# Optimization experiments

Hardware: AMD Instinct MI355X
Metric: run time of the kernel (lower is better)

## Reference

```python
import jax, jax.numpy as jnp
import numpy as np

B, T, E, H = 256, 1024, 32, 128
N_OBS = 1048576
N_OBS_VOCAB = 11  # n_lands + 2
N_ACT_VOCAB = 5   # n_acts + 2


def setup_inputs() -> dict:
    key = jax.random.key(0)
    ks = jax.random.split(key, 10)
    obs_ids = jax.random.randint(ks[0], (N_OBS,), 0, N_OBS_VOCAB)
    obs_slot = jnp.sort(jax.random.randint(ks[1], (N_OBS,), 0, B * T))
    action_ids = jax.random.randint(ks[2], (B, T), 0, N_ACT_VOCAB)
    is_action = jax.random.bernoulli(ks[3], 0.5, (B, T))
    lengths = jax.random.randint(ks[4], (B,), T // 4, T + 1)
    input_lengths = jnp.sort(lengths)[::-1]  # pack_padded_sequence requires descending
    s = 1.0 / np.sqrt(H)
    action_emb = jax.random.normal(ks[5], (N_ACT_VOCAB, E), jnp.float32)
    obs_emb = jax.random.normal(ks[6], (N_OBS_VOCAB, E), jnp.float32)
    W_ih = jax.random.uniform(ks[7], (4 * H, E), jnp.float32, -s, s)
    W_hh = jax.random.uniform(ks[8], (4 * H, H), jnp.float32, -s, s)
    b_ih = jax.random.uniform(ks[9], (4 * H,), jnp.float32, -s, s)
    b_hh = jnp.zeros((4 * H,), jnp.float32)
    return dict(obs_ids=obs_ids, obs_slot=obs_slot, action_ids=action_ids,
                is_action=is_action, input_lengths=input_lengths,
                action_emb=action_emb, obs_emb=obs_emb,
                W_ih=W_ih, W_hh=W_hh, b_ih=b_ih, b_hh=b_hh)


def _embed(obs_ids, obs_slot, action_ids, is_action, action_emb, obs_emb):
    # fused ragged embedding-bag: gather + segment-sum over observation lists
    obs_sum = jax.ops.segment_sum(obs_emb[obs_ids], obs_slot, num_segments=B * T)
    obs_sum = obs_sum.reshape(B, T, E)
    act = action_emb[action_ids]  # [B,T,E]
    return jnp.where(is_action[..., None], act, obs_sum)


def _lstm(embedded, input_lengths, W_ih, W_hh, b_ih, b_hh):
    mask = (jnp.arange(T)[None, :] < input_lengths[:, None])  # [B,T]
    xs = jnp.swapaxes(embedded, 0, 1)                         # [T,B,E]
    ms = mask.T[..., None].astype(embedded.dtype)             # [T,B,1]

    def step(carry, inp):
        h, c = carry
        x, m = inp
        gates = x @ W_ih.T + h @ W_hh.T + (b_ih + b_hh)  # [B,4H]
        i, f, g, o = jnp.split(gates, 4, axis=-1)        # torch gate order i,f,g,o
        i, f, o = jax.nn.sigmoid(i), jax.nn.sigmoid(f), jax.nn.sigmoid(o)
        g = jnp.tanh(g)
        c_new = f * c + i * g
        h_new = o * jnp.tanh(c_new)
        h = m * h_new + (1.0 - m) * h  # frozen past length (packed semantics)
        c = m * c_new + (1.0 - m) * c
        return (h, c), h * m           # pad_packed zero-pads past length

    h0 = jnp.zeros((B, H), embedded.dtype)
    c0 = jnp.zeros((B, H), embedded.dtype)
    (hN, cN), outs = jax.lax.scan(step, (h0, c0), (xs, ms))
    return jnp.swapaxes(outs, 0, 1), hN[None], cN[None]  # outputs [B,T,H], h/c [1,B,H]


def reference(obs_ids, obs_slot, action_ids, is_action, input_lengths,
              action_emb, obs_emb, W_ih, W_hh, b_ih, b_hh):
    embedded = _embed(obs_ids, obs_slot, action_ids, is_action, action_emb, obs_emb)
    outputs, h, c = _lstm(embedded, input_lengths, W_ih, W_hh, b_ih, b_hh)
    return outputs, h, c, embedded
```

## Files before the change

### kernel.cpp

```cpp
#include <hip/hip_runtime.h>

#define B_ 256
#define T_ 1024
#define E_ 32
#define H_ 128
#define NOBS_ 1048576
#define L2E 1.4426950408889634f
#define CLM 30.0f

#define HROW 144
#define HBUF (4 * HROW)

typedef __attribute__((ext_vector_type(8))) short bf16x8;
typedef __attribute__((ext_vector_type(4))) float f32x4;
typedef __attribute__((ext_vector_type(4))) int   i32x4;

#define LDS_BARRIER() asm volatile("s_waitcnt lgkmcnt(0)\n\ts_barrier" ::: "memory")

__device__ __forceinline__ short f2bf(float x) {
    unsigned u = __float_as_uint(x);
    unsigned r = u + 0x7FFFu + ((u >> 16) & 1u);
    return (short)(r >> 16);
}

__device__ __forceinline__ bf16x8 pack8(float4 lo, float4 hi) {
    int x0, x1, x2, x3;
    asm("v_cvt_pk_bf16_f32 %0, %1, %2" : "=v"(x0) : "v"(lo.x), "v"(lo.y));
    asm("v_cvt_pk_bf16_f32 %0, %1, %2" : "=v"(x1) : "v"(lo.z), "v"(lo.w));
    asm("v_cvt_pk_bf16_f32 %0, %1, %2" : "=v"(x2) : "v"(hi.x), "v"(hi.y));
    asm("v_cvt_pk_bf16_f32 %0, %1, %2" : "=v"(x3) : "v"(hi.z), "v"(hi.w));
    i32x4 xi; xi[0] = x0; xi[1] = x1; xi[2] = x2; xi[3] = x3;
    return __builtin_bit_cast(bf16x8, xi);
}

__global__ void embed_kernel(const int* __restrict__ obs_ids,
                             const int* __restrict__ obs_slot,
                             const int* __restrict__ action_ids,
                             const int* __restrict__ is_action,
                             const float* __restrict__ action_emb,
                             const float* __restrict__ obs_emb,
                             float* __restrict__ embedded,
                             unsigned short* __restrict__ xbf) {
    __shared__ float s_act[5 * E_];
    __shared__ float s_obs[11 * E_];
    for (int i = threadIdx.x; i < 5 * E_; i += blockDim.x) s_act[i] = action_emb[i];
    for (int i = threadIdx.x; i < 11 * E_; i += blockDim.x) s_obs[i] = obs_emb[i];
    __syncthreads();

    int s = blockIdx.x * blockDim.x + threadIdx.x;
    if (s >= B_ * T_) return;

    float acc[E_];
    if (is_action[s]) {
        int a = action_ids[s];
        #pragma unroll
        for (int e = 0; e < E_; e++) acc[e] = s_act[a * E_ + e];
    } else {
        #pragma unroll
        for (int e = 0; e < E_; e++) acc[e] = 0.0f;
        int lo = 0, hi = NOBS_;
        while (lo < hi) {
            int mid = (lo + hi) >> 1;
            if (obs_slot[mid] < s) lo = mid + 1; else hi = mid;
        }
        int j = lo;
        while (j < NOBS_ && obs_slot[j] == s) {
            int id = obs_ids[j];
            #pragma unroll
            for (int e = 0; e < E_; e++) acc[e] += s_obs[id * E_ + e];
            j++;
        }
    }
    float4* dst = (float4*)(embedded + (size_t)s * E_);
    #pragma unroll
    for (int q = 0; q < E_ / 4; q++) {
        float4 v; v.x = acc[4*q]; v.y = acc[4*q+1]; v.z = acc[4*q+2]; v.w = acc[4*q+3];
        dst[q] = v;
    }
    if (xbf) {
        unsigned short tmp[E_];
        #pragma unroll
        for (int e = 0; e < E_; e++) tmp[e] = (unsigned short)f2bf(acc[e]);
        int4* d2 = (int4*)(xbf + (size_t)s * E_);
        #pragma unroll
        for (int q = 0; q < E_ / 8; q++) d2[q] = ((const int4*)tmp)[q];
    }
}

template<bool BF16X>
__launch_bounds__(512, 2)
__global__ void lstm_kernel(const float* __restrict__ embedded,
                            const unsigned short* __restrict__ xbf,
                            const int* __restrict__ lengths,
                            const float* __restrict__ W_ih,
                            const float* __restrict__ W_hh,
                            const float* __restrict__ b_ih,
                            const float* __restrict__ b_hh,
                            float* __restrict__ outputs,
                            float* __restrict__ h_out,
                            float* __restrict__ c_out) {
    __shared__ __align__(16) char h_lds[2 * HBUF];

    const int tid  = threadIdx.x;
    const int lane = tid & 63;
    const int wave = tid >> 6;
    const int row0 = blockIdx.x * 4;

    const int col16  = (wave << 4) + (lane & 15);
    const int kgrp8  = (lane >> 4) * 8;
    const int kgrp16 = (lane >> 4) * 16;
    const int brow   = (lane & 15) >> 2;
    const int g_own  = lane >> 4;

    bf16x8 wx[4]; f32x4 biasv[4]; i32x4 wh[4][2]; float dq[4];
    #pragma unroll
    for (int gt = 0; gt < 4; gt++) {
        const float scale = (gt == 2) ? (2.0f * L2E) : L2E;
        const int gcol = gt * H_ + col16;
        {
            const float* p = W_ih + (size_t)gcol * E_ + kgrp8;
            bf16x8 v;
            #pragma unroll
            for (int j = 0; j < 8; j++) v[j] = f2bf(p[j] * scale);
            wx[gt] = v;
        }
        biasv[gt] = (f32x4)((b_ih[gcol] + b_hh[gcol]) * scale);

        const float* q = W_hh + (size_t)gcol * H_;
        float m = 0.0f;
        #pragma unroll
        for (int t2 = 0; t2 < 2; t2++)
            #pragma unroll
            for (int j = 0; j < 16; j++)
                m = fmaxf(m, fabsf(q[t2 * 64 + kgrp16 + j]));
        m = fmaxf(m, __shfl_xor(m, 16));
        m = fmaxf(m, __shfl_xor(m, 32));
        const float s = 127.0f / m;
        dq[gt] = scale * m * (1.0f / (127.0f * 127.0f));
        #pragma unroll
        for (int t2 = 0; t2 < 2; t2++) {
            i32x4 v;
            #pragma unroll
            for (int d = 0; d < 4; d++) {
                int word = 0;
                #pragma unroll
                for (int b2 = 0; b2 < 4; b2++) {
                    int qi = (int)rintf(q[t2 * 64 + kgrp16 + d * 4 + b2] * s);
                    word |= (qi & 0xFF) << (b2 * 8);
                }
                v[d] = word;
            }
            wh[gt][t2] = v;
        }
    }

    const int len = lengths[row0 + g_own];
    float cr = 0.0f, hr = 0.0f;

    const unsigned short* xpb = xbf + ((size_t)(row0 + brow) * T_) * E_ + kgrp8;
    const float*          xpf = embedded + ((size_t)(row0 + brow) * T_) * E_ + kgrp8;

    const int rbase = brow * HROW + kgrp16;
    const int wofs  = g_own * HROW + col16;
    float* const out_base = outputs + (size_t)(row0 + g_own) * T_ * H_ + col16;

    for (int i = tid; i < 2 * HBUF; i += 512) h_lds[i] = 0;
    __syncthreads();

    int4 xfA, xfB;
    float4 flA, fhA, flB, fhB;
    auto loadx = [&](int t, int4& xi4, float4& fl, float4& fh) {
        if (BF16X) {
            xi4 = *(const int4*)(xpb + (size_t)t * E_);
        } else {
            fl = *(const float4*)(xpf + (size_t)t * E_);
            fh = *(const float4*)(xpf + (size_t)t * E_ + 4);
        }
    };
    auto mkfrag = [&](const int4& xi4, const float4& fl, const float4& fh) -> bf16x8 {
        if (BF16X) return __builtin_bit_cast(bf16x8, xi4);
        return pack8(fl, fh);
    };

    loadx(0, xfA, flA, fhA);
    loadx(1, xfB, flB, fhB);
    f32x4 accfA[4], accfB[4];
    {
        bf16x8 xa = mkfrag(xfA, flA, fhA);
        #pragma unroll
        for (int gt = 0; gt < 4; gt++)
            accfA[gt] = __builtin_amdgcn_mfma_f32_16x16x32_bf16(xa, wx[gt], biasv[gt], 0, 0, 0);
    }

    auto step = [&](int t, int RD, int WR,
                    f32x4* accf_cur, f32x4* accf_nxt,
                    const int4& xf_nx, const float4& fl_nx, const float4& fh_nx,
                    int4& xf_pf, float4& fl_pf, float4& fh_pf,
                    bool PF1, bool PF2) {
        i32x4 ah0 = *(const i32x4*)&h_lds[RD + rbase];
        i32x4 ah1 = *(const i32x4*)&h_lds[RD + rbase + 64];

        if (PF2) loadx(t + 2, xf_pf, fl_pf, fh_pf);

        __builtin_amdgcn_s_setprio(1);
        i32x4 acci[4];
        #pragma unroll
        for (int gt = 0; gt < 4; gt++)
            acci[gt] = __builtin_amdgcn_mfma_i32_16x16x64_i8(ah0, wh[gt][0], (i32x4)0, 0, 0, 0);
        #pragma unroll
        for (int gt = 0; gt < 4; gt++)
            acci[gt] = __builtin_amdgcn_mfma_i32_16x16x64_i8(ah1, wh[gt][1], acci[gt], 0, 0, 0);
        if (PF1) {
            bf16x8 xa = mkfrag(xf_nx, fl_nx, fh_nx);
            #pragma unroll
            for (int gt = 0; gt < 4; gt++)
                accf_nxt[gt] = __builtin_amdgcn_mfma_f32_16x16x32_bf16(xa, wx[gt], biasv[gt], 0, 0, 0);
        }
        __builtin_amdgcn_s_setprio(0);

        float a_i = fmaf((float)acci[0][0], dq[0], accf_cur[0][0]);
        float a_f = fmaf((float)acci[1][0], dq[1], accf_cur[1][0]);
        float a_g = fmaf((float)acci[2][0], dq[2], accf_cur[2][0]);
        float a_o = fmaf((float)acci[3][0], dq[3], accf_cur[3][0]);
        float Ai = exp2f(fminf(-a_i, CLM));
        float Af = exp2f(fminf(-a_f, CLM));
        float Eg = exp2f(fminf(a_g, CLM));
        float pAi = 1.0f + Ai, pAf = 1.0f + Af, pEg = Eg + 1.0f;
        float D  = pAi * pEg;
        float R  = __builtin_amdgcn_rcpf(D * pAf);
        float f_ = D * R;
        float ig = (Eg - 1.0f) * pAf * R;
        float c_new = fmaf(f_, cr, ig);
        float Ec = exp2f(fminf(c_new * (2.0f * L2E), CLM));
        float Ao = exp2f(fminf(-a_o, CLM));
        float Rh = __builtin_amdgcn_rcpf((1.0f + Ao) * (Ec + 1.0f));
        float h_new = (Ec - 1.0f) * Rh;
        bool m = (t < len);
        cr = m ? c_new : cr;
        hr = m ? h_new : hr;

        unsigned qb = __float_as_uint(fmaf(hr, 127.0f, 12582912.0f));
        h_lds[WR + wofs] = (char)qb;
        out_base[(size_t)t * H_] = m ? h_new : 0.0f;

        LDS_BARRIER();
    };

    for (int t = 0; t < T_ - 2; t += 2) {
        step(t,     0,    HBUF, accfA, accfB, xfB, flB, fhB, xfA, flA, fhA, true, true);
        step(t + 1, HBUF, 0,    accfB, accfA, xfA, flA, fhA, xfB, flB, fhB, true, t + 3 < T_);
    }
    step(T_ - 2, 0,    HBUF, accfA, accfB, xfB, flB, fhB, xfA, flA, fhA, true,  false);
    step(T_ - 1, HBUF, 0,    accfB, accfA, xfA, flA, fhA, xfB, flB, fhB, false, false);

    h_out[(size_t)(row0 + g_own) * H_ + col16] = hr;
    c_out[(size_t)(row0 + g_own) * H_ + col16] = cr;
}

extern "C" void kernel_launch(void* const* d_in, const int* in_sizes, int n_in,
                              void* d_out, int out_size, void* d_ws, size_t ws_size,
                              hipStream_t stream) {
    const int*   obs_ids       = (const int*)d_in[0];
    const int*   obs_slot      = (const int*)d_in[1];
    const int*   action_ids    = (const int*)d_in[2];
    const int*   is_action     = (const int*)d_in[3];
    const int*   input_lengths = (const int*)d_in[4];
    const float* action_emb    = (const float*)d_in[5];
    const float* obs_emb       = (const float*)d_in[6];
    const float* W_ih          = (const float*)d_in[7];
    const float* W_hh          = (const float*)d_in[8];
    const float* b_ih          = (const float*)d_in[9];
    const float* b_hh          = (const float*)d_in[10];

    float* out      = (float*)d_out;
    float* outputs  = out;
    float* h_out    = out + (size_t)B_ * T_ * H_;
    float* c_out    = h_out + (size_t)B_ * H_;
    float* embedded = c_out + (size_t)B_ * H_;

    const size_t xbf_bytes = (size_t)B_ * T_ * E_ * sizeof(unsigned short);
    const bool use_bf16x = (ws_size >= xbf_bytes);
    unsigned short* xbf = use_bf16x ? (unsigned short*)d_ws : nullptr;

    hipLaunchKernelGGL(embed_kernel, dim3((B_ * T_ + 255) / 256), dim3(256), 0, stream,
                       obs_ids, obs_slot, action_ids, is_action, action_emb, obs_emb,
                       embedded, xbf);

    if (use_bf16x) {
        hipLaunchKernelGGL((lstm_kernel<true>), dim3(B_ / 4), dim3(512), 0, stream,
                           embedded, xbf, input_lengths, W_ih, W_hh, b_ih, b_hh,
                           outputs, h_out, c_out);
    } else {
        hipLaunchKernelGGL((lstm_kernel<false>), dim3(B_ / 4), dim3(512), 0, stream,
                           embedded, xbf, input_lengths, W_ih, W_hh, b_ih, b_hh,
                           outputs, h_out, c_out);
    }
}
```

Before: 487.3 us.

## Run one batch row per LSTM block instead of four

Changes the LSTM kernel so that each 512-thread block handles a single batch row, launching 256 blocks instead of 64. This spreads the serial recurrence across more CUs to use more of the GPU. It also removes the software pipelining of the input projection, which is now computed inside the same step. Only 16 lanes per wave write results, so most MFMA rows do wasted work, and the per-step latency chain now includes the x-projection MFMAs.

```diff
diff --git a/kernel.cpp b/kernel.cpp
--- a/kernel.cpp
+++ b/kernel.cpp
@@ -8,8 +8,7 @@
 #define L2E 1.4426950408889634f
 #define CLM 30.0f
 
-#define HROW 144
-#define HBUF (4 * HROW)
+#define HR1 144
 
 typedef __attribute__((ext_vector_type(8))) short bf16x8;
 typedef __attribute__((ext_vector_type(4))) float f32x4;
@@ -88,29 +87,27 @@
 }
 
 template<bool BF16X>
-__launch_bounds__(512, 2)
-__global__ void lstm_kernel(const float* __restrict__ embedded,
-                            const unsigned short* __restrict__ xbf,
-                            const int* __restrict__ lengths,
-                            const float* __restrict__ W_ih,
-                            const float* __restrict__ W_hh,
-                            const float* __restrict__ b_ih,
-                            const float* __restrict__ b_hh,
-                            float* __restrict__ outputs,
-                            float* __restrict__ h_out,
-                            float* __restrict__ c_out) {
-    __shared__ __align__(16) char h_lds[2 * HBUF];
+__launch_bounds__(512)
+__global__ void lstm1_kernel(const float* __restrict__ embedded,
+                             const unsigned short* __restrict__ xbf,
+                             const int* __restrict__ lengths,
+                             const float* __restrict__ W_ih,
+                             const float* __restrict__ W_hh,
+                             const float* __restrict__ b_ih,
+                             const float* __restrict__ b_hh,
+                             float* __restrict__ outputs,
+                             float* __restrict__ h_out,
+                             float* __restrict__ c_out) {
+    __shared__ __align__(16) char h_lds[2 * HR1];
 
     const int tid  = threadIdx.x;
     const int lane = tid & 63;
     const int wave = tid >> 6;
-    const int row0 = blockIdx.x * 4;
+    const int row  = blockIdx.x;
 
     const int col16  = (wave << 4) + (lane & 15);
     const int kgrp8  = (lane >> 4) * 8;
     const int kgrp16 = (lane >> 4) * 16;
-    const int brow   = (lane & 15) >> 2;
-    const int g_own  = lane >> 4;
 
     bf16x8 wx[4]; f32x4 biasv[4]; i32x4 wh[4][2]; float dq[4];
     #pragma unroll
@@ -154,17 +151,14 @@
         }
     }
 
-    const int len = lengths[row0 + g_own];
+    const int len = lengths[row];
     float cr = 0.0f, hr = 0.0f;
 
-    const unsigned short* xpb = xbf + ((size_t)(row0 + brow) * T_) * E_ + kgrp8;
-    const float*          xpf = embedded + ((size_t)(row0 + brow) * T_) * E_ + kgrp8;
-
-    const int rbase = brow * HROW + kgrp16;
-    const int wofs  = g_own * HROW + col16;
-    float* const out_base = outputs + (size_t)(row0 + g_own) * T_ * H_ + col16;
-
-    for (int i = tid; i < 2 * HBUF; i += 512) h_lds[i] = 0;
+    const unsigned short* xpb = xbf + (size_t)row * T_ * E_ + kgrp8;
+    const float*          xpf = embedded + (size_t)row * T_ * E_ + kgrp8;
+    float* const out_base = outputs + (size_t)row * T_ * H_ + col16;
+
+    for (int i = tid; i < 2 * HR1; i += 512) h_lds[i] = 0;
     __syncthreads();
 
     int4 xfA, xfB;
@@ -184,44 +178,35 @@
 
     loadx(0, xfA, flA, fhA);
     loadx(1, xfB, flB, fhB);
-    f32x4 accfA[4], accfB[4];
-    {
-        bf16x8 xa = mkfrag(xfA, flA, fhA);
+
+    int RD = 0;
+    for (int t = 0; t < T_; ++t) {
+        const int cur = t & 1;
+        i32x4 ah0 = *(const i32x4*)&h_lds[RD + kgrp16];
+        i32x4 ah1 = *(const i32x4*)&h_lds[RD + 64 + kgrp16];
+        bf16x8 xa = mkfrag(cur ? xfB : xfA, cur ? flB : flA, cur ? fhB : fhA);
+        if (t + 2 < T_) {
+            if (cur) loadx(t + 2, xfB, flB, fhB);
+            else     loadx(t + 2, xfA, flA, fhA);
+        }
+
+        __builtin_amdgcn_s_setprio(1);
+        f32x4 accf[4]; i32x4 acci[4];
         #pragma unroll
         for (int gt = 0; gt < 4; gt++)
-            accfA[gt] = __builtin_amdgcn_mfma_f32_16x16x32_bf16(xa, wx[gt], biasv[gt], 0, 0, 0);
-    }
-
-    auto step = [&](int t, int RD, int WR,
-                    f32x4* accf_cur, f32x4* accf_nxt,
-                    const int4& xf_nx, const float4& fl_nx, const float4& fh_nx,
-                    int4& xf_pf, float4& fl_pf, float4& fh_pf,
-                    bool PF1, bool PF2) {
-        i32x4 ah0 = *(const i32x4*)&h_lds[RD + rbase];
-        i32x4 ah1 = *(const i32x4*)&h_lds[RD + rbase + 64];
-
-        if (PF2) loadx(t + 2, xf_pf, fl_pf, fh_pf);
-
-        __builtin_amdgcn_s_setprio(1);
-        i32x4 acci[4];
+            accf[gt] = __builtin_amdgcn_mfma_f32_16x16x32_bf16(xa, wx[gt], biasv[gt], 0, 0, 0);
         #pragma unroll
         for (int gt = 0; gt < 4; gt++)
             acci[gt] = __builtin_amdgcn_mfma_i32_16x16x64_i8(ah0, wh[gt][0], (i32x4)0, 0, 0, 0);
         #pragma unroll
         for (int gt = 0; gt < 4; gt++)
             acci[gt] = __builtin_amdgcn_mfma_i32_16x16x64_i8(ah1, wh[gt][1], acci[gt], 0, 0, 0);
-        if (PF1) {
-            bf16x8 xa = mkfrag(xf_nx, fl_nx, fh_nx);
-            #pragma unroll
-            for (int gt = 0; gt < 4; gt++)
-                accf_nxt[gt] = __builtin_amdgcn_mfma_f32_16x16x32_bf16(xa, wx[gt], biasv[gt], 0, 0, 0);
-        }
         __builtin_amdgcn_s_setprio(0);
 
-        float a_i = fmaf((float)acci[0][0], dq[0], accf_cur[0][0]);
-        float a_f = fmaf((float)acci[1][0], dq[1], accf_cur[1][0]);
-        float a_g = fmaf((float)acci[2][0], dq[2], accf_cur[2][0]);
-        float a_o = fmaf((float)acci[3][0], dq[3], accf_cur[3][0]);
+        float a_i = fmaf((float)acci[0][0], dq[0], accf[0][0]);
+        float a_f = fmaf((float)acci[1][0], dq[1], accf[1][0]);
+        float a_g = fmaf((float)acci[2][0], dq[2], accf[2][0]);
+        float a_o = fmaf((float)acci[3][0], dq[3], accf[3][0]);
         float Ai = exp2f(fminf(-a_i, CLM));
         float Af = exp2f(fminf(-a_f, CLM));
         float Eg = exp2f(fminf(a_g, CLM));
@@ -239,22 +224,20 @@
         cr = m ? c_new : cr;
         hr = m ? h_new : hr;
 
-        unsigned qb = __float_as_uint(fmaf(hr, 127.0f, 12582912.0f));
-        h_lds[WR + wofs] = (char)qb;
-        out_base[(size_t)t * H_] = m ? h_new : 0.0f;
-
+        const int WR = RD ^ HR1;
+        if (lane < 16) {
+            unsigned qb = __float_as_uint(fmaf(hr, 127.0f, 12582912.0f));
+            h_lds[WR + col16] = (char)qb;
+            out_base[(size_t)t * H_] = m ? h_new : 0.0f;
+        }
+        RD = WR;
         LDS_BARRIER();
-    };
-
-    for (int t = 0; t < T_ - 2; t += 2) {
-        step(t,     0,    HBUF, accfA, accfB, xfB, flB, fhB, xfA, flA, fhA, true, true);
-        step(t + 1, HBUF, 0,    accfB, accfA, xfA, flA, fhA, xfB, flB, fhB, true, t + 3 < T_);
-    }
-    step(T_ - 2, 0,    HBUF, accfA, accfB, xfB, flB, fhB, xfA, flA, fhA, true,  false);
-    step(T_ - 1, HBUF, 0,    accfB, accfA, xfA, flA, fhA, xfB, flB, fhB, false, false);
-
-    h_out[(size_t)(row0 + g_own) * H_ + col16] = hr;
-    c_out[(size_t)(row0 + g_own) * H_ + col16] = cr;
+    }
+
+    if (lane < 16) {
+        h_out[(size_t)row * H_ + col16] = hr;
+        c_out[(size_t)row * H_ + col16] = cr;
+    }
 }
 
 extern "C" void kernel_launch(void* const* d_in, const int* in_sizes, int n_in,
@@ -287,11 +270,11 @@
                        embedded, xbf);
 
     if (use_bf16x) {
-        hipLaunchKernelGGL((lstm_kernel<true>), dim3(B_ / 4), dim3(512), 0, stream,
+        hipLaunchKernelGGL((lstm1_kernel<true>), dim3(B_), dim3(512), 0, stream,
                            embedded, xbf, input_lengths, W_ih, W_hh, b_ih, b_hh,
                            outputs, h_out, c_out);
     } else {
-        hipLaunchKernelGGL((lstm_kernel<false>), dim3(B_ / 4), dim3(512), 0, stream,
+        hipLaunchKernelGGL((lstm1_kernel<false>), dim3(B_), dim3(512), 0, stream,
                            embedded, xbf, input_lengths, W_ih, W_hh, b_ih, b_hh,
                            outputs, h_out, c_out);
     }
```

Measured after the change: 747.9 us. +53.5%, slower.

## Batch input projection over four timesteps per MFMA using all accumulator rows

Applied to the files above, without the earlier changes.

The input projection MFMA previously produced 16 rows but only row 0 of each accumulator was used, so one x-projection ran per timestep. Each lane now loads the input for timestep offset (lane&3), so one bf16 MFMA yields the projections for four consecutive timesteps, indexed by accf[gt][i]. This cuts the x-projection MFMAs and global loads per step by four and prefetches eight steps ahead. The trade-off is that the projection is no longer overlapped inside the recurrent step and accumulators are held across four steps.

```diff
diff --git a/kernel.cpp b/kernel.cpp
--- a/kernel.cpp
+++ b/kernel.cpp
@@ -110,6 +110,7 @@
     const int kgrp8  = (lane >> 4) * 8;
     const int kgrp16 = (lane >> 4) * 16;
     const int brow   = (lane & 15) >> 2;
+    const int toff   = (lane & 15) & 3;
     const int g_own  = lane >> 4;
 
     bf16x8 wx[4]; f32x4 biasv[4]; i32x4 wh[4][2]; float dq[4];
@@ -157,8 +158,8 @@
     const int len = lengths[row0 + g_own];
     float cr = 0.0f, hr = 0.0f;
 
-    const unsigned short* xpb = xbf + ((size_t)(row0 + brow) * T_) * E_ + kgrp8;
-    const float*          xpf = embedded + ((size_t)(row0 + brow) * T_) * E_ + kgrp8;
+    const unsigned short* xpb = xbf + ((size_t)(row0 + brow) * T_ + toff) * E_ + kgrp8;
+    const float*          xpf = embedded + ((size_t)(row0 + brow) * T_ + toff) * E_ + kgrp8;
 
     const int rbase = brow * HROW + kgrp16;
     const int wofs  = g_own * HROW + col16;
@@ -167,14 +168,14 @@
     for (int i = tid; i < 2 * HBUF; i += 512) h_lds[i] = 0;
     __syncthreads();
 
-    int4 xfA, xfB;
-    float4 flA, fhA, flB, fhB;
-    auto loadx = [&](int t, int4& xi4, float4& fl, float4& fh) {
+    int4 xf0, xf1;
+    float4 fl0, fh0, fl1, fh1;
+    auto loadx = [&](int tg, int4& xi4, float4& fl, float4& fh) {
         if (BF16X) {
-            xi4 = *(const int4*)(xpb + (size_t)t * E_);
+            xi4 = *(const int4*)(xpb + (size_t)tg * E_);
         } else {
-            fl = *(const float4*)(xpf + (size_t)t * E_);
-            fh = *(const float4*)(xpf + (size_t)t * E_ + 4);
+            fl = *(const float4*)(xpf + (size_t)tg * E_);
+            fh = *(const float4*)(xpf + (size_t)tg * E_ + 4);
         }
     };
     auto mkfrag = [&](const int4& xi4, const float4& fl, const float4& fh) -> bf16x8 {
@@ -182,76 +183,72 @@
         return pack8(fl, fh);
     };
 
-    loadx(0, xfA, flA, fhA);
-    loadx(1, xfB, flB, fhB);
-    f32x4 accfA[4], accfB[4];
-    {
-        bf16x8 xa = mkfrag(xfA, flA, fhA);
+    loadx(0, xf0, fl0, fh0);
+    loadx(4, xf1, fl1, fh1);
+
+    auto group = [&](int tg, const int4& xf_u, const float4& fl_u, const float4& fh_u,
+                     int4& xf_p, float4& fl_p, float4& fh_p, bool PF) {
+        bf16x8 xa = mkfrag(xf_u, fl_u, fh_u);
+        f32x4 accf[4];
+        __builtin_amdgcn_s_setprio(1);
         #pragma unroll
         for (int gt = 0; gt < 4; gt++)
-            accfA[gt] = __builtin_amdgcn_mfma_f32_16x16x32_bf16(xa, wx[gt], biasv[gt], 0, 0, 0);
-    }
-
-    auto step = [&](int t, int RD, int WR,
-                    f32x4* accf_cur, f32x4* accf_nxt,
-                    const int4& xf_nx, const float4& fl_nx, const float4& fh_nx,
-                    int4& xf_pf, float4& fl_pf, float4& fh_pf,
-                    bool PF1, bool PF2) {
-        i32x4 ah0 = *(const i32x4*)&h_lds[RD + rbase];
-        i32x4 ah1 = *(const i32x4*)&h_lds[RD + rbase + 64];
-
-        if (PF2) loadx(t + 2, xf_pf, fl_pf, fh_pf);
-
-        __builtin_amdgcn_s_setprio(1);
-        i32x4 acci[4];
-        #pragma unroll
-        for (int gt = 0; gt < 4; gt++)
-            acci[gt] = __builtin_amdgcn_mfma_i32_16x16x64_i8(ah0, wh[gt][0], (i32x4)0, 0, 0, 0);
-        #pragma unroll
-        for (int gt = 0; gt < 4; gt++)
-            acci[gt] = __builtin_amdgcn_mfma_i32_16x16x64_i8(ah1, wh[gt][1], acci[gt], 0, 0, 0);
-        if (PF1) {
-            bf16x8 xa = mkfrag(xf_nx, fl_nx, fh_nx);
+            accf[gt] = __builtin_amdgcn_mfma_f32_16x16x32_bf16(xa, wx[gt], biasv[gt], 0, 0, 0);
+        __builtin_amdgcn_s_setprio(0);
+        if (PF) loadx(tg + 8, xf_p, fl_p, fh_p);
+
+        #pragma unroll
+        for (int i = 0; i < 4; i++) {
+            const int t  = tg + i;
+            const int RD = (i & 1) ? HBUF : 0;
+            const int WR = RD ^ HBUF;
+
+            i32x4 ah0 = *(const i32x4*)&h_lds[RD + rbase];
+            i32x4 ah1 = *(const i32x4*)&h_lds[RD + rbase + 64];
+
+            __builtin_amdgcn_s_setprio(1);
+            i32x4 acci[4];
             #pragma unroll
             for (int gt = 0; gt < 4; gt++)
-                accf_nxt[gt] = __builtin_amdgcn_mfma_f32_16x16x32_bf16(xa, wx[gt], biasv[gt], 0, 0, 0);
-        }
-        __builtin_amdgcn_s_setprio(0);
-
-        float a_i = fmaf((float)acci[0][0], dq[0], accf_cur[0][0]);
-        float a_f = fmaf((float)acci[1][0], dq[1], accf_cur[1][0]);
-        float a_g = fmaf((float)acci[2][0], dq[2], accf_cur[2][0]);
-        float a_o = fmaf((float)acci[3][0], dq[3], accf_cur[3][0]);
-        float Ai = exp2f(fminf(-a_i, CLM));
-        float Af = exp2f(fminf(-a_f, CLM));
-        float Eg = exp2f(fminf(a_g, CLM));
-        float pAi = 1.0f + Ai, pAf = 1.0f + Af, pEg = Eg + 1.0f;
-        float D  = pAi * pEg;
-        float R  = __builtin_amdgcn_rcpf(D * pAf);
-        float f_ = D * R;
-        float ig = (Eg - 1.0f) * pAf * R;
-        float c_new = fmaf(f_, cr, ig);
-        float Ec = exp2f(fminf(c_new * (2.0f * L2E), CLM));
-        float Ao = exp2f(fminf(-a_o, CLM));
-        float Rh = __builtin_amdgcn_rcpf((1.0f + Ao) * (Ec + 1.0f));
-        float h_new = (Ec - 1.0f) * Rh;
-        bool m = (t < len);
-        cr = m ? c_new : cr;
-        hr = m ? h_new : hr;
-
-        unsigned qb = __float_as_uint(fmaf(hr, 127.0f, 12582912.0f));
-        h_lds[WR + wofs] = (char)qb;
-        out_base[(size_t)t * H_] = m ? h_new : 0.0f;
-
-        LDS_BARRIER();
+                acci[gt] = __builtin_amdgcn_mfma_i32_16x16x64_i8(ah0, wh[gt][0], (i32x4)0, 0, 0, 0);
+            #pragma unroll
+            for (int gt = 0; gt < 4; gt++)
+                acci[gt] = __builtin_amdgcn_mfma_i32_16x16x64_i8(ah1, wh[gt][1], acci[gt], 0, 0, 0);
+            __builtin_amdgcn_s_setprio(0);
+
+            float a_i = fmaf((float)acci[0][0], dq[0], accf[0][i]);
+            float a_f = fmaf((float)acci[1][0], dq[1], accf[1][i]);
+            float a_g = fmaf((float)acci[2][0], dq[2], accf[2][i]);
+            float a_o = fmaf((float)acci[3][0], dq[3], accf[3][i]);
+            float Ai = exp2f(fminf(-a_i, CLM));
+            float Af = exp2f(fminf(-a_f, CLM));
+            float Eg = exp2f(fminf(a_g, CLM));
+            float pAi = 1.0f + Ai, pAf = 1.0f + Af, pEg = Eg + 1.0f;
+            float D  = pAi * pEg;
+            float R  = __builtin_amdgcn_rcpf(D * pAf);
+            float f_ = D * R;
+            float ig = (Eg - 1.0f) * pAf * R;
+            float c_new = fmaf(f_, cr, ig);
+            float Ec = exp2f(fminf(c_new * (2.0f * L2E), CLM));
+            float Ao = exp2f(fminf(-a_o, CLM));
+            float Rh = __builtin_amdgcn_rcpf((1.0f + Ao) * (Ec + 1.0f));
+            float h_new = (Ec - 1.0f) * Rh;
+            bool m = (t < len);
+            cr = m ? c_new : cr;
+            hr = m ? h_new : hr;
+
+            unsigned qb = __float_as_uint(fmaf(hr, 127.0f, 12582912.0f));
+            h_lds[WR + wofs] = (char)qb;
+            out_base[(size_t)t * H_] = m ? h_new : 0.0f;
+
+            LDS_BARRIER();
+        }
     };
 
-    for (int t = 0; t < T_ - 2; t += 2) {
-        step(t,     0,    HBUF, accfA, accfB, xfB, flB, fhB, xfA, flA, fhA, true, true);
-        step(t + 1, HBUF, 0,    accfB, accfA, xfA, flA, fhA, xfB, flB, fhB, true, t + 3 < T_);
-    }
-    step(T_ - 2, 0,    HBUF, accfA, accfB, xfB, flB, fhB, xfA, flA, fhA, true,  false);
-    step(T_ - 1, HBUF, 0,    accfB, accfA, xfA, flA, fhA, xfB, flB, fhB, false, false);
+    for (int tg = 0; tg < T_; tg += 8) {
+        group(tg,     xf0, fl0, fh0, xf0, fl0, fh0, tg + 8 < T_);
+        group(tg + 4, xf1, fl1, fh1, xf1, fl1, fh1, tg + 12 < T_);
+    }
 
     h_out[(size_t)(row0 + g_own) * H_ + col16] = hr;
     c_out[(size_t)(row0 + g_own) * H_ + col16] = cr;
```

After: 440.2 us, median of 2. 1.11x faster.
